# Optimization experiments

Hardware: AMD Instinct MI355X
Metric: run time of the kernel (lower is better)

## Reference

```python
import jax, jax.numpy as jnp
import numpy as np

PAD_IDX = 1  # word2vec key_to_index['<PAD>'] / padding_idx in the original
VOCAB, EMBED, HIDDEN, SEQ = 100000, 300, 512, 1024


def setup_inputs() -> dict:
    key = jax.random.key(0)
    k = jax.random.split(key, 8)
    s = 1.0 / np.sqrt(HIDDEN)  # PyTorch LSTM init scale
    return {
        "input_seq": jax.random.randint(k[0], (1, SEQ), 0, VOCAB, dtype=jnp.int64)
                     if jax.config.jax_enable_x64 else
                     jax.random.randint(k[0], (1, SEQ), 0, VOCAB, dtype=jnp.int32),
        "h0": jnp.zeros((1, 1, HIDDEN), jnp.float32),
        "c0": jnp.zeros((1, 1, HIDDEN), jnp.float32),
        "emb": jax.random.normal(k[1], (VOCAB, EMBED), jnp.float32),  # frozen word2vec table
        "W_ih": jax.random.uniform(k[2], (4 * HIDDEN, EMBED), jnp.float32, -s, s),
        "W_hh": jax.random.uniform(k[3], (4 * HIDDEN, HIDDEN), jnp.float32, -s, s),
        "b_ih": jax.random.uniform(k[4], (4 * HIDDEN,), jnp.float32, -s, s),
        "b_hh": jax.random.uniform(k[5], (4 * HIDDEN,), jnp.float32, -s, s),
    }


def _lstm_scan(xs, is_pad, h, c, W_ih, W_hh, b_ih, b_hh):
    # xs: [S, E]; PAD steps leave (h, c, out) untouched, matching the `continue`.
    x_gates = xs @ W_ih.T + b_ih  # [S, 4H] -- hoist input projection out of the scan
    H = h.shape[-1]

    def step(carry, inp):
        h, c, out = carry
        xg, pad = inp
        g = xg + h @ W_hh.T + b_hh                 # [4H], PyTorch gate order i,f,g,o
        i, f, gg, o = jnp.split(g, 4)
        c_new = jax.nn.sigmoid(f) * c + jax.nn.sigmoid(i) * jnp.tanh(gg)
        h_new = jax.nn.sigmoid(o) * jnp.tanh(c_new)
        h = jnp.where(pad, h, h_new)
        c = jnp.where(pad, c, c_new)
        out = jnp.where(pad, out, h_new)
        return (h, c, out), None

    (h, c, out), _ = jax.lax.scan(step, (h, c, jnp.zeros(H, xs.dtype)), (x_gates, is_pad))
    return h, c, out


def reference(input_seq, h0, c0, emb, W_ih, W_hh, b_ih, b_hh):
    tokens = input_seq[0]                 # batch==1 in the original
    xs = emb[tokens]                      # [S, E] embedding gather (fused into recurrence)
    is_pad = tokens == PAD_IDX
    h, c, out = _lstm_scan(xs, is_pad, h0[0, 0], c0[0, 0], W_ih, W_hh, b_ih, b_hh)
    # original returns output=None if every token is PAD; here out stays zeros.
    return (out[None, None, :], (h[None, None, :], c[None, None, :]))
```

## Files before the change

### kernel.cpp

```cpp
#include <hip/hip_runtime.h>
#include <math.h>

#define SEQ    1024
#define EMBED  300
#define HIDDEN 512
#define G4     2048
#define NB     32
#define NBLK   256
#define TPB    1024
#define UPB    (HIDDEN/NB)
#define PAD_IDX 1
#define SENT   0x7FC00BADu

#define HSLOT  32
#define HROW   (NB * HSLOT)

__device__ float        g_xg[SEQ * G4];
__device__ float        g_hp[(SEQ + 1) * HROW];
__device__ unsigned int g_done;
__device__ float        g_sink;

__device__ __forceinline__ float sigmoidf_(float x) {
    return 1.f / (1.f + __expf(-x));
}
__device__ __forceinline__ float tanhf_(float x) {
    return 1.f - 2.f / (__expf(2.f * x) + 1.f);
}

#define DPP_ADD(v, ctrl)                                                      \
    (v) += __int_as_float(__builtin_amdgcn_update_dpp(                        \
        0, __float_as_int(v), (ctrl), 0xf, 0xf, true))

__global__ __launch_bounds__(256) void xgates_kernel(
    const int* __restrict__ seq, const float* __restrict__ h0,
    const float* __restrict__ emb, const float* __restrict__ W_ih,
    const float* __restrict__ b_ih, const float* __restrict__ b_hh)
{
    const int bx = blockIdx.x, tid = threadIdx.x;

    if (bx == 0 && tid == 0) g_done = 0u;
    for (int i = bx * 256 + tid; i < (SEQ + 1) * HROW; i += 256 * 256) {
        int step = i >> 10, slot = i & (HROW - 1);
        int blk = slot >> 5, k = slot & (HSLOT - 1);
        float v = __uint_as_float(SENT);
        if (step == 0 && k < UPB) v = h0[blk * UPB + k];
        g_hp[i] = v;
    }

    const int t_tile = bx >> 1, k_half = bx & 1;
    const int t0 = t_tile * 8;

    __shared__ int tok_s[8];
    __shared__ __align__(16) float embt[8][304];

    if (tid < 8) tok_s[tid] = seq[t0 + tid];
    __syncthreads();
    for (int idx = tid; idx < 8 * EMBED; idx += 256) {
        int tt = idx / EMBED;
        int e  = idx - tt * EMBED;
        embt[tt][e] = emb[(size_t)tok_s[tt] * EMBED + e];
    }
    __syncthreads();

    const int kbase = k_half * 1024 + tid;
    const float4* wr0 = (const float4*)(W_ih + (size_t)(kbase      ) * EMBED);
    const float4* wr1 = (const float4*)(W_ih + (size_t)(kbase + 256) * EMBED);
    const float4* wr2 = (const float4*)(W_ih + (size_t)(kbase + 512) * EMBED);
    const float4* wr3 = (const float4*)(W_ih + (size_t)(kbase + 768) * EMBED);

    float acc[4][8];
    #pragma unroll
    for (int kk = 0; kk < 4; kk++)
        #pragma unroll
        for (int tt = 0; tt < 8; tt++) acc[kk][tt] = 0.f;

    for (int e4 = 0; e4 < EMBED / 4; e4++) {
        float4 em[8];
        #pragma unroll
        for (int tt = 0; tt < 8; tt++)
            em[tt] = *(const float4*)&embt[tt][e4 * 4];
        float4 w[4];
        w[0] = wr0[e4]; w[1] = wr1[e4]; w[2] = wr2[e4]; w[3] = wr3[e4];
        #pragma unroll
        for (int kk = 0; kk < 4; kk++) {
            #pragma unroll
            for (int tt = 0; tt < 8; tt++) {
                float a = acc[kk][tt];
                a = fmaf(w[kk].x, em[tt].x, a);
                a = fmaf(w[kk].y, em[tt].y, a);
                a = fmaf(w[kk].z, em[tt].z, a);
                a = fmaf(w[kk].w, em[tt].w, a);
                acc[kk][tt] = a;
            }
        }
    }
    #pragma unroll
    for (int kk = 0; kk < 4; kk++) {
        int k = kbase + kk * 256;
        float bias = b_ih[k] + b_hh[k];
        #pragma unroll
        for (int tt = 0; tt < 8; tt++)
            g_xg[(size_t)(t0 + tt) * G4 + k] = acc[kk][tt] + bias;
    }
}

__global__ __launch_bounds__(TPB, 1) void lstm_kernel(
    const int* __restrict__ seq, const float* __restrict__ h0,
    const float* __restrict__ c0, const float* __restrict__ Whh,
    const float* __restrict__ emb, float* __restrict__ out)
{
    const int b = blockIdx.x, tid = threadIdx.x;

    if (b >= NB) {
        if (tid < 256) {
            float a0 = 1.0f + b, a1 = 2.0f, a2 = 3.0f, a3 = 4.0f;
            for (;;) {
                #pragma unroll
                for (int i = 0; i < 128; i++) {
                    a0 = fmaf(a0, 1.000001f, 0.5f);
                    a1 = fmaf(a1, 0.999999f, 0.25f);
                    a2 = fmaf(a2, 1.0000005f, a0);
                    a3 = fmaf(a3, 0.9999995f, a1);
                }
                if (__hip_atomic_load(&g_done, __ATOMIC_RELAXED,
                                      __HIP_MEMORY_SCOPE_AGENT)) break;
            }
            if (a0 == 1234.5678f && a1 == a2) g_sink = a3;
        } else if (tid < 320 && ((b & 3) == 0)) {
            const float4* p = (const float4*)emb;
            const size_t mask = (1u << 22) - 1;
            size_t base = (size_t)(b - NB) * 131072 + (tid & 63);
            float acc = 0.f;
            for (;;) {
                float4 v0 = p[(base          ) & mask];
                float4 v1 = p[(base +  1 * 64) & mask];
                float4 v2 = p[(base +  2 * 64) & mask];
                float4 v3 = p[(base +  3 * 64) & mask];
                float4 v4 = p[(base +  4 * 64) & mask];
                float4 v5 = p[(base +  5 * 64) & mask];
                float4 v6 = p[(base +  6 * 64) & mask];
                float4 v7 = p[(base +  7 * 64) & mask];
                acc += v0.x + v1.y + v2.z + v3.w + v4.x + v5.y + v6.z + v7.w;
                base += 8 * 64;
                if (__hip_atomic_load(&g_done, __ATOMIC_RELAXED,
                                      __HIP_MEMORY_SCOPE_AGENT)) break;
            }
            if (acc == 1234.5678f) g_sink = acc;
        }
        return;
    }

    const int u = tid >> 6;
    const int lane = tid & 63;
    const int g = lane >> 4, c = lane & 15;
    const int R = g * HIDDEN + b * UPB + u;

    const float* wrow = Whh + (size_t)R * HIDDEN + c * 32;
    float4 wreg[8];
    #pragma unroll
    for (int i = 0; i < 8; i++) {
        int off = (4 * i + 4 * c) & 31;
        wreg[i] = *(const float4*)(wrow + off);
    }

    __shared__ __align__(16) float h_lds[2][HIDDEN];
    __shared__ float hpub[UPB];
    __shared__ int   tok_lds[SEQ];

    for (int i = tid; i < SEQ; i += TPB) tok_lds[i] = seq[i];

    const bool owner = (lane == 0);
    float c_state = 0.f, h_state = 0.f;
    if (owner) {
        c_state = c0[b * UPB + u];
        h_state = h0[b * UPB + u];
    }
    __syncthreads();

    int np = 0;
    bool any = false;

    for (int t = 0; t < SEQ; t++) {
        int tok = tok_lds[t];
        if (tok == PAD_IDX) continue;
        any = true;

        float xi = 0.f, xf = 0.f, xgg = 0.f, xo = 0.f;
        if (owner) {
            const float* xr = g_xg + (size_t)t * G4 + b * UPB + u;
            xi  = xr[0];
            xf  = xr[HIDDEN];
            xgg = xr[2 * HIDDEN];
            xo  = xr[3 * HIDDEN];
        }

        if (tid < 256) {
            const int blk = tid >> 3, j = tid & 7;
            const unsigned long long* hb = (const unsigned long long*)
                (g_hp + (size_t)np * HROW + blk * HSLOT);
            unsigned long long v;
            do {
                v = __hip_atomic_load(hb + j, __ATOMIC_RELAXED,
                                      __HIP_MEMORY_SCOPE_AGENT);
            } while ((unsigned)v == SENT || (unsigned)(v >> 32) == SENT);
            *(unsigned long long*)&h_lds[np & 1][blk * UPB + 2 * j] = v;
        }
        __syncthreads();

        const float* hc = h_lds[np & 1] + c * 32;
        float4 a4 = {0.f, 0.f, 0.f, 0.f};
        #pragma unroll
        for (int i = 0; i < 8; i++) {
            int off = (4 * i + 4 * c) & 31;
            float4 h4 = *(const float4*)(hc + off);
            a4.x = fmaf(wreg[i].x, h4.x, a4.x);
            a4.y = fmaf(wreg[i].y, h4.y, a4.y);
            a4.z = fmaf(wreg[i].z, h4.z, a4.z);
            a4.w = fmaf(wreg[i].w, h4.w, a4.w);
        }
        float dotv = (a4.x + a4.y) + (a4.z + a4.w);
        DPP_ADD(dotv, 0xB1);
        DPP_ADD(dotv, 0x4E);
        DPP_ADD(dotv, 0x141);
        DPP_ADD(dotv, 0x140);

        float d1 = __shfl(dotv, 16);
        float d2 = __shfl(dotv, 32);
        float d3 = __shfl(dotv, 48);

        if (owner) {
            float iv = sigmoidf_(xi  + dotv);
            float fv = sigmoidf_(xf  + d1);
            float gv = tanhf_   (xgg + d2);
            float ov = sigmoidf_(xo  + d3);
            c_state = fv * c_state + iv * gv;
            h_state = ov * tanhf_(c_state);
            hpub[u] = h_state;
        }
        __syncthreads();

        if (tid < UPB) {
            __hip_atomic_store(
                (unsigned*)(g_hp + (size_t)(np + 1) * HROW + b * HSLOT) + tid,
                __float_as_uint(hpub[tid]),
                __ATOMIC_RELAXED, __HIP_MEMORY_SCOPE_AGENT);
        }
        np++;
    }

    if (owner) {
        int uo = b * UPB + u;
        out[uo]              = any ? h_state : 0.f;
        out[HIDDEN + uo]     = h_state;
        out[2 * HIDDEN + uo] = c_state;
    }
    if (b == 0 && tid == 0) {
        __hip_atomic_store(&g_done, 1u, __ATOMIC_RELAXED,
                           __HIP_MEMORY_SCOPE_AGENT);
    }
}

extern "C" void kernel_launch(void* const* d_in, const int* in_sizes, int n_in,
                              void* d_out, int out_size, void* d_ws, size_t ws_size,
                              hipStream_t stream)
{
    const int*   seq  = (const int*)  d_in[0];
    const float* h0   = (const float*)d_in[1];
    const float* c0   = (const float*)d_in[2];
    const float* emb  = (const float*)d_in[3];
    const float* W_ih = (const float*)d_in[4];
    const float* W_hh = (const float*)d_in[5];
    const float* b_ih = (const float*)d_in[6];
    const float* b_hh = (const float*)d_in[7];
    float* out = (float*)d_out;

    hipLaunchKernelGGL(xgates_kernel, dim3(256), dim3(256), 0, stream,
                       seq, h0, emb, W_ih, b_ih, b_hh);

    void* args[] = { (void*)&seq, (void*)&h0, (void*)&c0, (void*)&W_hh,
                     (void*)&emb, (void*)&out };
    hipLaunchCooperativeKernel((const void*)lstm_kernel, dim3(NBLK), dim3(TPB),
                               args, 0, stream);
}
```

Measured before the change: 2.217 ms.

## Spread LSTM recurrence over 128 smaller blocks and publish hidden state directly

The recurrent kernel now uses 128 blocks of 256 threads, each owning 4 hidden units, instead of 32 blocks of 1024 threads owning 16. Each owner lane writes its new h straight to the global exchange buffer, which drops the shared staging array and one block barrier per step. The polling loop now issues four atomic loads per iteration, and the dummy blocks that streamed the embedding table are removed. Using more blocks should shorten each block's barrier and compute path, but every step now has four times as many blocks polling and gathering the full hidden vector from global memory.

```diff
diff --git a/kernel.cpp b/kernel.cpp
--- a/kernel.cpp
+++ b/kernel.cpp
@@ -5,9 +5,9 @@
 #define EMBED  300
 #define HIDDEN 512
 #define G4     2048
-#define NB     32
+#define NB     128
 #define NBLK   256
-#define TPB    1024
+#define TPB    256
 #define UPB    (HIDDEN/NB)
 #define PAD_IDX 1
 #define SENT   0x7FC00BADu
@@ -40,7 +40,7 @@
 
     if (bx == 0 && tid == 0) g_done = 0u;
     for (int i = bx * 256 + tid; i < (SEQ + 1) * HROW; i += 256 * 256) {
-        int step = i >> 10, slot = i & (HROW - 1);
+        int step = i >> 12, slot = i & (HROW - 1);
         int blk = slot >> 5, k = slot & (HSLOT - 1);
         float v = __uint_as_float(SENT);
         if (step == 0 && k < UPB) v = h0[blk * UPB + k];
@@ -107,13 +107,13 @@
 __global__ __launch_bounds__(TPB, 1) void lstm_kernel(
     const int* __restrict__ seq, const float* __restrict__ h0,
     const float* __restrict__ c0, const float* __restrict__ Whh,
-    const float* __restrict__ emb, float* __restrict__ out)
+    float* __restrict__ out)
 {
     const int b = blockIdx.x, tid = threadIdx.x;
 
     if (b >= NB) {
-        if (tid < 256) {
-            float a0 = 1.0f + b, a1 = 2.0f, a2 = 3.0f, a3 = 4.0f;
+        if (tid < 128) {
+            float a0 = 1.0f + tid, a1 = 2.0f, a2 = 3.0f, a3 = 4.0f;
             for (;;) {
                 #pragma unroll
                 for (int i = 0; i < 128; i++) {
@@ -126,26 +126,6 @@
                                       __HIP_MEMORY_SCOPE_AGENT)) break;
             }
             if (a0 == 1234.5678f && a1 == a2) g_sink = a3;
-        } else if (tid < 320 && ((b & 3) == 0)) {
-            const float4* p = (const float4*)emb;
-            const size_t mask = (1u << 22) - 1;
-            size_t base = (size_t)(b - NB) * 131072 + (tid & 63);
-            float acc = 0.f;
-            for (;;) {
-                float4 v0 = p[(base          ) & mask];
-                float4 v1 = p[(base +  1 * 64) & mask];
-                float4 v2 = p[(base +  2 * 64) & mask];
-                float4 v3 = p[(base +  3 * 64) & mask];
-                float4 v4 = p[(base +  4 * 64) & mask];
-                float4 v5 = p[(base +  5 * 64) & mask];
-                float4 v6 = p[(base +  6 * 64) & mask];
-                float4 v7 = p[(base +  7 * 64) & mask];
-                acc += v0.x + v1.y + v2.z + v3.w + v4.x + v5.y + v6.z + v7.w;
-                base += 8 * 64;
-                if (__hip_atomic_load(&g_done, __ATOMIC_RELAXED,
-                                      __HIP_MEMORY_SCOPE_AGENT)) break;
-            }
-            if (acc == 1234.5678f) g_sink = acc;
         }
         return;
     }
@@ -164,8 +144,7 @@
     }
 
     __shared__ __align__(16) float h_lds[2][HIDDEN];
-    __shared__ float hpub[UPB];
-    __shared__ int   tok_lds[SEQ];
+    __shared__ int tok_lds[SEQ];
 
     for (int i = tid; i < SEQ; i += TPB) tok_lds[i] = seq[i];
 
@@ -194,15 +173,25 @@
             xo  = xr[3 * HIDDEN];
         }
 
-        if (tid < 256) {
-            const int blk = tid >> 3, j = tid & 7;
+        {
+            const int blk = tid >> 1, j = tid & 1;
             const unsigned long long* hb = (const unsigned long long*)
-                (g_hp + (size_t)np * HROW + blk * HSLOT);
+                (g_hp + (size_t)np * HROW + blk * HSLOT) + j;
             unsigned long long v;
-            do {
-                v = __hip_atomic_load(hb + j, __ATOMIC_RELAXED,
-                                      __HIP_MEMORY_SCOPE_AGENT);
-            } while ((unsigned)v == SENT || (unsigned)(v >> 32) == SENT);
+            for (;;) {
+                unsigned long long p0 = __hip_atomic_load(hb, __ATOMIC_RELAXED,
+                                            __HIP_MEMORY_SCOPE_AGENT);
+                unsigned long long p1 = __hip_atomic_load(hb, __ATOMIC_RELAXED,
+                                            __HIP_MEMORY_SCOPE_AGENT);
+                unsigned long long p2 = __hip_atomic_load(hb, __ATOMIC_RELAXED,
+                                            __HIP_MEMORY_SCOPE_AGENT);
+                unsigned long long p3 = __hip_atomic_load(hb, __ATOMIC_RELAXED,
+                                            __HIP_MEMORY_SCOPE_AGENT);
+                if ((unsigned)p0 != SENT && (unsigned)(p0 >> 32) != SENT) { v = p0; break; }
+                if ((unsigned)p1 != SENT && (unsigned)(p1 >> 32) != SENT) { v = p1; break; }
+                if ((unsigned)p2 != SENT && (unsigned)(p2 >> 32) != SENT) { v = p2; break; }
+                if ((unsigned)p3 != SENT && (unsigned)(p3 >> 32) != SENT) { v = p3; break; }
+            }
             *(unsigned long long*)&h_lds[np & 1][blk * UPB + 2 * j] = v;
         }
         __syncthreads();
@@ -235,14 +224,9 @@
             float ov = sigmoidf_(xo  + d3);
             c_state = fv * c_state + iv * gv;
             h_state = ov * tanhf_(c_state);
-            hpub[u] = h_state;
-        }
-        __syncthreads();
-
-        if (tid < UPB) {
             __hip_atomic_store(
-                (unsigned*)(g_hp + (size_t)(np + 1) * HROW + b * HSLOT) + tid,
-                __float_as_uint(hpub[tid]),
+                (unsigned*)(g_hp + (size_t)(np + 1) * HROW + b * HSLOT) + u,
+                __float_as_uint(h_state),
                 __ATOMIC_RELAXED, __HIP_MEMORY_SCOPE_AGENT);
         }
         np++;
@@ -278,7 +262,7 @@
                        seq, h0, emb, W_ih, b_ih, b_hh);
 
     void* args[] = { (void*)&seq, (void*)&h0, (void*)&c0, (void*)&W_hh,
-                     (void*)&emb, (void*)&out };
+                     (void*)&out };
     hipLaunchCooperativeKernel((const void*)lstm_kernel, dim3(NBLK), dim3(TPB),
                                args, 0, stream);
 }
```

Result: slower. 2.362 ms (+6.5%).
